# Kernel tuning notes

Hardware: AMD Instinct MI355X
Metric: run time of the kernel (lower is better)

The kernel has to match this reference:

```python
import jax, jax.numpy as jnp
import numpy as np

N = 50000      # nodes
E = 600000     # edges (avg degree 12)
DIN, DE, DH = 17, 1, 128
L, H, C = 3, 4, 32   # layers, heads, per-head channels (DH = H*C)
NEG_SLOPE = 0.2


def setup_inputs() -> dict:
    key = jax.random.key(0)
    ks = jax.random.split(key, 18)
    rn = lambda k, s, sc: jax.random.normal(k, s, jnp.float32) * sc
    return {
        "x": rn(ks[0], (N, DIN), 1.0),
        "edge_index": jax.random.randint(ks[1], (2, E), 0, N, dtype=jnp.int64),
        "edge_attr": rn(ks[2], (E, DE), 1.0),
        "enc_node_w": rn(ks[3], (DIN, DH), 1.0 / np.sqrt(DIN)),
        "enc_node_b": jnp.zeros((DH,), jnp.float32),
        "enc_edge_w": rn(ks[4], (DE, DH), 1.0),
        "enc_edge_b": jnp.zeros((DH,), jnp.float32),
        "lin_w": rn(ks[5], (L, DH, DH), 1.0 / np.sqrt(DH)),
        "lin_edge_w": rn(ks[6], (L, DH, DH), 1.0 / np.sqrt(DH)),
        "att_src": rn(ks[7], (L, H, C), 1.0 / np.sqrt(C)),
        "att_dst": rn(ks[8], (L, H, C), 1.0 / np.sqrt(C)),
        "att_edge": rn(ks[9], (L, H, C), 1.0 / np.sqrt(C)),
        "gat_bias": jnp.zeros((L, DH), jnp.float32),
        "dec_w1": rn(ks[10], (DH, DH), 1.0 / np.sqrt(DH)),
        "dec_b1": jnp.zeros((DH,), jnp.float32),
        "dec_w2": rn(ks[11], (DH, 2), 1.0 / np.sqrt(DH)),
        "dec_b2": jnp.zeros((2,), jnp.float32),
    }


def _gat_layer(x, src, dst, e_attr, W, We, a_src, a_dst, a_edge, bias):
    """PyG GATConv, concat=True, dropout in eval mode (identity).
    x: [N,DH], src/dst: [E2] (self-loops already appended), e_attr: [E2,DH]."""
    n = x.shape[0]
    h = (x @ W).reshape(n, H, C)                       # [N,H,C]
    alpha_src = jnp.einsum('nhc,hc->nh', h, a_src)     # [N,H]
    alpha_dst = jnp.einsum('nhc,hc->nh', h, a_dst)
    e = (e_attr @ We).reshape(-1, H, C)                # [E2,H,C]
    alpha_e = jnp.einsum('ehc,hc->eh', e, a_edge)      # [E2,H]
    logits = jax.nn.leaky_relu(alpha_src[src] + alpha_dst[dst] + alpha_e, NEG_SLOPE)
    # segment softmax over edges grouped by destination node
    mx = jax.ops.segment_max(logits, dst, num_segments=n)          # [N,H]
    num = jnp.exp(logits - mx[dst])                                # [E2,H]
    den = jax.ops.segment_sum(num, dst, num_segments=n)            # [N,H]
    alpha = num / (den[dst] + 1e-16)                               # [E2,H]
    msg = h[src] * alpha[:, :, None]                               # [E2,H,C]
    out = jax.ops.segment_sum(msg, dst, num_segments=n)            # [N,H,C]
    return out.reshape(n, H * C) + bias


def reference(x, edge_index, edge_attr,
              enc_node_w, enc_node_b, enc_edge_w, enc_edge_b,
              lin_w, lin_edge_w, att_src, att_dst, att_edge, gat_bias,
              dec_w1, dec_b1, dec_w2, dec_b2):
    n = x.shape[0]
    src, dst = edge_index[0], edge_index[1]
    h = x @ enc_node_w + enc_node_b                    # node encoder
    ea = edge_attr @ enc_edge_w + enc_edge_b           # edge encoder [E,DH]
    # add_self_loops with fill_value='mean': self-loop attr = mean of incoming edge attrs
    ea_sum = jax.ops.segment_sum(ea, dst, num_segments=n)
    cnt = jax.ops.segment_sum(jnp.ones((ea.shape[0],), ea.dtype), dst, num_segments=n)
    loop_attr = ea_sum / jnp.maximum(cnt, 1.0)[:, None]
    loop_idx = jnp.arange(n, dtype=src.dtype)
    src_f = jnp.concatenate([src, loop_idx])
    dst_f = jnp.concatenate([dst, loop_idx])
    ea_f = jnp.concatenate([ea, loop_attr], axis=0)    # [E+N,DH]
    for l in range(L):
        h = _gat_layer(h, src_f, dst_f, ea_f,
                       lin_w[l], lin_edge_w[l],
                       att_src[l], att_dst[l], att_edge[l], gat_bias[l])
        h = jax.nn.elu(h)
    h = jax.nn.relu(h @ dec_w1 + dec_b1)
    return h @ dec_w2 + dec_b2                          # [N,2]
```

## Files before the change

kernel.cpp:

```cpp
#include <hip/hip_runtime.h>
#include <hip/hip_fp16.h>
#include <math.h>

#define DIN 17
#define DH  128
#define NH  4
#define CC  32
#define NL  3
#define NEG 0.2f

#define CSTRIDE 64

typedef _Float16 hf;
typedef _Float16 f16x8 __attribute__((ext_vector_type(8)));
typedef float    f32x4 __attribute__((ext_vector_type(4)));

#define NT 9

__global__ void __launch_bounds__(256) prep_kernel(
        const float* __restrict__ ew, const float* __restrict__ eb,
        const float* __restrict__ We, const float* __restrict__ ae,
        const float* __restrict__ lin_w, const float* __restrict__ dec_w1,
        const float* __restrict__ att_src, const float* __restrict__ att_dst,
        float* __restrict__ pq, hf* __restrict__ wfrag,
        int* __restrict__ cnt, int N) {
    int b = blockIdx.x, tid = threadIdx.x;
    if (b < 12) {
        if (tid < 64) {
            int l = b >> 2, h = b & 3;
            const float* Wel = We + l * DH * DH;
            const float* ael = ae + l * DH + h * CC;
            float p = 0.f, q = 0.f;
            for (int d = tid; d < DH; d += 64) {
                const float* row = Wel + d * DH + h * CC;
                float wp = 0.f;
                for (int c = 0; c < CC; ++c) wp += row[c] * ael[c];
                p += ew[d] * wp;
                q += eb[d] * wp;
            }
            for (int o = 32; o > 0; o >>= 1) {
                p += __shfl_down(p, o, 64);
                q += __shfl_down(q, o, 64);
            }
            if (tid == 0) { pq[b * 2 + 0] = p; pq[b * 2 + 1] = q; }
        }
    } else if (b < 48) {
        int bb = b - 12;
        int m = bb / NT, nt = bb % NT;
        int lane = tid & 63, kk = tid >> 6;
        int colr = lane & 15, kg = lane >> 4;
        hf* dst = wfrag + ((((size_t)bb * 4 + kk) * 64) + lane) * 8;
        if (nt < 8) {
            const float* src = (m < 3) ? (lin_w + (size_t)m * DH * DH) : dec_w1;
            #pragma unroll
            for (int jj = 0; jj < 8; ++jj) {
                int k = kk * 32 + kg * 8 + jj;
                dst[jj] = (hf)src[k * DH + nt * 16 + colr];
            }
        } else if (m < 3 && colr < 8) {
            int hh = colr >> 1;
            const float* W = lin_w + (size_t)m * DH * DH;
            const float* a = ((colr & 1) ? att_dst : att_src) + m * DH + hh * CC;
            #pragma unroll
            for (int jj = 0; jj < 8; ++jj) {
                int k = kk * 32 + kg * 8 + jj;
                float s = 0.f;
                #pragma unroll
                for (int c = 0; c < CC; ++c) s += W[k * DH + hh * CC + c] * a[c];
                dst[jj] = (hf)s;
            }
        } else {
            #pragma unroll
            for (int jj = 0; jj < 8; ++jj) dst[jj] = (hf)0.f;
        }
    } else {
        int i = (b - 48) * 256 + tid;
        if (i < N) cnt[i] = 0;
    }
}

__global__ void __launch_bounds__(256) rank_enc_kernel(
        const int* __restrict__ ei, const float* __restrict__ ea,
        int* __restrict__ cnt, int2* __restrict__ csr,
        const float* __restrict__ x, const float* __restrict__ Wn,
        const float* __restrict__ bn, hf* __restrict__ h16,
        int E, int N, int EB) {
    __shared__ float wl[DIN][DH];
    __shared__ float xs[32][DIN];
    int tid = threadIdx.x;
    if ((int)blockIdx.x < EB) {
        int e = blockIdx.x * 256 + tid;
        if (e >= E) return;
        int d = ei[E + e];
        int rk = atomicAdd(&cnt[d], 1);
        if (rk < CSTRIDE) {
            int2 p; p.x = ei[e]; p.y = __float_as_int(ea[e]);
            csr[(size_t)d * CSTRIDE + rk] = p;
        }
    } else {
        int row0 = (blockIdx.x - EB) * 32;
        for (int i = tid; i < DIN * DH; i += 256) wl[i / DH][i % DH] = Wn[i];
        for (int i = tid; i < 32 * DIN; i += 256) {
            int r = i / DIN, k = i % DIN;
            int rr = row0 + r; if (rr > N - 1) rr = N - 1;
            xs[r][k] = x[(size_t)rr * DIN + k];
        }
        __syncthreads();
        int c = tid & 127;
        int g = tid >> 7;
        float bias = bn[c];
        #pragma unroll
        for (int r = 0; r < 16; ++r) {
            int row = row0 + g * 16 + r;
            if (row >= N) break;
            float acc = bias;
            #pragma unroll
            for (int k = 0; k < DIN; ++k) acc += xs[g * 16 + r][k] * wl[k][c];
            h16[(size_t)row * DH + c] = (hf)acc;
        }
    }
}

__device__ __forceinline__ void ln_body(
        const hf* __restrict__ h16, const hf* __restrict__ wfrag,
        __half* __restrict__ h1h, float* __restrict__ as_, float* __restrict__ ad_,
        int N, int blk) {
    __shared__ uint4 lds[64 * 16];
    int tid = threadIdx.x;
    int row0 = blk * 64;
    #pragma unroll
    for (int i = 0; i < 4; ++i) {
        int idx = tid + i * 256;
        int r = idx >> 4, ch = idx & 15;
        int gr = row0 + r; if (gr > N - 1) gr = N - 1;
        lds[r * 16 + (ch ^ (r & 7))] = ((const uint4*)(h16 + (size_t)gr * DH))[ch];
    }
    __syncthreads();

    int w = tid >> 6, lane = tid & 63;
    int colr = lane & 15, kg = lane >> 4;
    int lrow = w * 16 + colr;

    f16x8 afr[4];
    #pragma unroll
    for (int kk = 0; kk < 4; ++kk) {
        int ch = (kk * 4 + kg) ^ (colr & 7);
        afr[kk] = *(const f16x8*)&lds[lrow * 16 + ch];
    }

    f32x4 acc[NT];
    #pragma unroll
    for (int nt = 0; nt < NT; ++nt) acc[nt] = (f32x4){0.f, 0.f, 0.f, 0.f};

    const f16x8* wf = (const f16x8*)wfrag;
    #pragma unroll
    for (int nt = 0; nt < NT; ++nt) {
        #pragma unroll
        for (int kk = 0; kk < 4; ++kk) {
            f16x8 bfr = wf[(size_t)(nt * 4 + kk) * 64 + lane];
            acc[nt] = __builtin_amdgcn_mfma_f32_16x16x32_f16(afr[kk], bfr, acc[nt], 0, 0, 0);
        }
    }

    #pragma unroll
    for (int r = 0; r < 4; ++r) {
        int grow = row0 + w * 16 + kg * 4 + r;
        if (grow < N) {
            #pragma unroll
            for (int nt = 0; nt < 8; ++nt)
                h1h[(size_t)grow * DH + nt * 16 + colr] = (__half)(float)acc[nt][r];
        }
    }
    if (colr < 8) {
        int id = colr, hh = id >> 1;
        #pragma unroll
        for (int r = 0; r < 4; ++r) {
            int grow = row0 + w * 16 + kg * 4 + r;
            if (grow < N) {
                float v = (float)acc[8][r];
                if (id & 1) ad_[grow * NH + hh] = v;
                else        as_[grow * NH + hh] = v;
            }
        }
    }
}

__global__ void __launch_bounds__(256) layer_node(
        const hf* __restrict__ h16, const hf* __restrict__ wfrag,
        __half* __restrict__ h1h, float* __restrict__ as_, float* __restrict__ ad_,
        int N) {
    ln_body(h16, wfrag, h1h, as_, ad_, N, blockIdx.x);
}

__global__ void __launch_bounds__(256) agg_kernel(
        const __half* __restrict__ h1h, const float* __restrict__ as_,
        const float* __restrict__ ad_,
        const int* __restrict__ cnt,
        const int2* __restrict__ csr,
        const float* __restrict__ pql, const float* __restrict__ bias,
        hf* __restrict__ hout, int N) {
    int n = blockIdx.x * 4 + (threadIdx.x >> 6);
    if (n >= N) return;
    int lane = threadIdx.x & 63;
    int hd = lane >> 4;
    int c0 = lane * 2;
    size_t off = (size_t)n * CSTRIDE;
    int dgt = cnt[n];
    int dg = dgt < CSTRIDE ? dgt : CSTRIDE;
    float adn = ad_[n * NH + hd];
    float pa = pql[hd * 2 + 0], qa = pql[hd * 2 + 1];

    const __half2* h1v = (const __half2*)h1h;

    float denA = 0.f, a0A = 0.f, a1A = 0.f;
    float denB = 0.f, a0B = 0.f, a1B = 0.f;
    float asv = 0.f;

    int i = 0;
    for (; i + 8 <= dg; i += 8) {
        int2 e[8];
        #pragma unroll
        for (int j = 0; j < 8; ++j) e[j] = csr[off + i + j];
        __half2 q[8];
        #pragma unroll
        for (int j = 0; j < 8; ++j) q[j] = h1v[(size_t)e[j].x * 64 + lane];
        float s[8];
        #pragma unroll
        for (int j = 0; j < 8; ++j) s[j] = as_[e[j].x * NH + hd];
        #pragma unroll
        for (int j = 0; j < 8; ++j) {
            float a = __int_as_float(e[j].y);
            asv += a;
            float t = s[j] + adn + a * pa + qa;
            t = fmaxf(t, NEG * t);
            float nm = __expf(t);
            float2 g = __half22float2(q[j]);
            if (j & 1) { denB += nm; a0B = fmaf(nm, g.x, a0B); a1B = fmaf(nm, g.y, a1B); }
            else       { denA += nm; a0A = fmaf(nm, g.x, a0A); a1A = fmaf(nm, g.y, a1A); }
        }
    }
    for (; i + 4 <= dg; i += 4) {
        int2 e[4];
        #pragma unroll
        for (int j = 0; j < 4; ++j) e[j] = csr[off + i + j];
        __half2 q[4];
        #pragma unroll
        for (int j = 0; j < 4; ++j) q[j] = h1v[(size_t)e[j].x * 64 + lane];
        float s[4];
        #pragma unroll
        for (int j = 0; j < 4; ++j) s[j] = as_[e[j].x * NH + hd];
        #pragma unroll
        for (int j = 0; j < 4; ++j) {
            float a = __int_as_float(e[j].y);
            asv += a;
            float t = s[j] + adn + a * pa + qa;
            t = fmaxf(t, NEG * t);
            float nm = __expf(t);
            float2 g = __half22float2(q[j]);
            if (j & 1) { denB += nm; a0B = fmaf(nm, g.x, a0B); a1B = fmaf(nm, g.y, a1B); }
            else       { denA += nm; a0A = fmaf(nm, g.x, a0A); a1A = fmaf(nm, g.y, a1A); }
        }
    }
    for (; i < dg; ++i) {
        int2 ep = csr[off + i];
        __half2 qs = h1v[(size_t)ep.x * 64 + lane];
        float a = __int_as_float(ep.y);
        asv += a;
        float lg = as_[ep.x * NH + hd] + adn + a * pa + qa;
        lg = fmaxf(lg, NEG * lg);
        float num = __expf(lg);
        float2 gs = __half22float2(qs);
        denA += num;
        a0A = fmaf(num, gs.x, a0A);
        a1A = fmaf(num, gs.y, a1A);
    }

    float sa = asv / fmaxf((float)dgt, 1.f);
    float ael = (dgt > 0) ? (sa * pa + qa) : 0.f;
    float l0 = as_[n * NH + hd] + adn + ael;
    l0 = fmaxf(l0, NEG * l0);
    float numS = __expf(l0);
    float2 hv = __half22float2(h1v[(size_t)n * 64 + lane]);

    float den = denA + denB + numS;
    float a0 = a0A + a0B + numS * hv.x;
    float a1 = a1A + a1B + numS * hv.y;
    float inv = 1.f / (den + 1e-16f);
    float o0 = a0 * inv + bias[c0];
    float o1 = a1 * inv + bias[c0 + 1];
    o0 = (o0 > 0.f) ? o0 : expm1f(o0);
    o1 = (o1 > 0.f) ? o1 : expm1f(o1);
    union { unsigned int u; hf hx[2]; } st;
    st.hx[0] = (hf)o0; st.hx[1] = (hf)o1;
    ((unsigned int*)hout)[(size_t)n * 64 + lane] = st.u;
}

__global__ void __launch_bounds__(256) dec_kernel(
        const hf* __restrict__ h16, const hf* __restrict__ wfrag,
        const float* __restrict__ b1, const float* __restrict__ w2,
        const float* __restrict__ b2, float* __restrict__ out, int N) {
    __shared__ uint4 lds[64 * 16];
    int tid = threadIdx.x;
    int row0 = blockIdx.x * 64;
    #pragma unroll
    for (int i = 0; i < 4; ++i) {
        int idx = tid + i * 256;
        int r = idx >> 4, ch = idx & 15;
        int gr = row0 + r; if (gr > N - 1) gr = N - 1;
        lds[r * 16 + (ch ^ (r & 7))] = ((const uint4*)(h16 + (size_t)gr * DH))[ch];
    }
    __syncthreads();

    int w = tid >> 6, lane = tid & 63;
    int colr = lane & 15, kg = lane >> 4;
    int lrow = w * 16 + colr;

    f16x8 afr[4];
    #pragma unroll
    for (int kk = 0; kk < 4; ++kk) {
        int ch = (kk * 4 + kg) ^ (colr & 7);
        afr[kk] = *(const f16x8*)&lds[lrow * 16 + ch];
    }

    f32x4 acc[8];
    #pragma unroll
    for (int nt = 0; nt < 8; ++nt) acc[nt] = (f32x4){0.f, 0.f, 0.f, 0.f};

    const f16x8* wf = (const f16x8*)wfrag;
    #pragma unroll
    for (int nt = 0; nt < 8; ++nt) {
        #pragma unroll
        for (int kk = 0; kk < 4; ++kk) {
            f16x8 bfr = wf[(size_t)(nt * 4 + kk) * 64 + lane];
            acc[nt] = __builtin_amdgcn_mfma_f32_16x16x32_f16(afr[kk], bfr, acc[nt], 0, 0, 0);
        }
    }

    float bb0 = b2[0], bb1 = b2[1];
    float b1v[8], w20[8], w21[8];
    #pragma unroll
    for (int nt = 0; nt < 8; ++nt) {
        int col = nt * 16 + colr;
        b1v[nt] = b1[col];
        w20[nt] = w2[col * 2 + 0];
        w21[nt] = w2[col * 2 + 1];
    }
    #pragma unroll
    for (int r = 0; r < 4; ++r) {
        float p0 = 0.f, p1 = 0.f;
        #pragma unroll
        for (int nt = 0; nt < 8; ++nt) {
            float hid = fmaxf((float)acc[nt][r] + b1v[nt], 0.f);
            p0 = fmaf(hid, w20[nt], p0);
            p1 = fmaf(hid, w21[nt], p1);
        }
        #pragma unroll
        for (int o = 1; o < 16; o <<= 1) {
            p0 += __shfl_xor(p0, o, 16);
            p1 += __shfl_xor(p1, o, 16);
        }
        int grow = row0 + w * 16 + kg * 4 + r;
        if (colr == 0 && grow < N) {
            out[grow * 2 + 0] = p0 + bb0;
            out[grow * 2 + 1] = p1 + bb1;
        }
    }
}

extern "C" void kernel_launch(void* const* d_in, const int* in_sizes, int n_in,
                              void* d_out, int out_size, void* d_ws, size_t ws_size,
                              hipStream_t stream) {
    const float* x          = (const float*)d_in[0];
    const int*   ei         = (const int*)d_in[1];
    const float* eattr      = (const float*)d_in[2];
    const float* enc_node_w = (const float*)d_in[3];
    const float* enc_node_b = (const float*)d_in[4];
    const float* enc_edge_w = (const float*)d_in[5];
    const float* enc_edge_b = (const float*)d_in[6];
    const float* lin_w      = (const float*)d_in[7];
    const float* lin_edge_w = (const float*)d_in[8];
    const float* att_src    = (const float*)d_in[9];
    const float* att_dst    = (const float*)d_in[10];
    const float* att_edge   = (const float*)d_in[11];
    const float* gat_bias   = (const float*)d_in[12];
    const float* dec_w1     = (const float*)d_in[13];
    const float* dec_b1     = (const float*)d_in[14];
    const float* dec_w2     = (const float*)d_in[15];
    const float* dec_b2     = (const float*)d_in[16];

    const int E = in_sizes[2];
    const int N = in_sizes[0] / DIN;

    char* w = (char*)d_ws;
    auto alloc = [&](size_t bytes) -> void* {
        void* p = (void*)w;
        w += (bytes + 511) & ~((size_t)511);
        return p;
    };
    hf*     h16   = (hf*)alloc((size_t)N * DH * 2);
    __half* h1h   = (__half*)alloc((size_t)N * DH * 2);
    float* as_    = (float*)alloc((size_t)N * NH * 4);
    float* ad_    = (float*)alloc((size_t)N * NH * 4);
    int*   cnt    = (int*)alloc((size_t)N * 4);
    int2*  csr    = (int2*)alloc((size_t)N * CSTRIDE * 8);
    float* pq     = (float*)alloc(NL * NH * 2 * 4);
    hf*    wfrag  = (hf*)alloc((size_t)4 * NT * 4 * 64 * 8 * 2);

    const int EB   = (E + 255) / 256;
    const int NB32 = (N + 31) / 32;
    const int AB   = (N + 255) / 256;
    const int LNB  = (N + 63) / 64;
    const size_t mstride = (size_t)NT * 4 * 64 * 8;

    prep_kernel<<<48 + AB, 256, 0, stream>>>(enc_edge_w, enc_edge_b, lin_edge_w, att_edge,
                                             lin_w, dec_w1, att_src, att_dst,
                                             pq, wfrag, cnt, N);
    rank_enc_kernel<<<EB + NB32, 256, 0, stream>>>(ei, eattr, cnt, csr,
                                                   x, enc_node_w, enc_node_b, h16,
                                                   E, N, EB);
    for (int l = 0; l < NL; ++l) {
        layer_node<<<LNB, 256, 0, stream>>>(h16, wfrag + (size_t)l * mstride,
                                            h1h, as_, ad_, N);
        agg_kernel<<<(N + 3) / 4, 256, 0, stream>>>(h1h, as_, ad_, cnt, csr,
                                                    pq + l * NH * 2, gat_bias + l * DH, h16, N);
    }
    dec_kernel<<<LNB, 256, 0, stream>>>(h16, wfrag + (size_t)3 * mstride,
                                        dec_b1, dec_w2, dec_b2,
                                        (float*)d_out, N);
}
```

Before: 305.4 us.

## Pack CSR entries into 32 bits and fuse prep with edge ranking kernel

Each CSR entry shrinks from an int2 (source index plus fp32 edge attribute) to one 32-bit word: a 16-bit source index and a half-precision edge attribute. This halves CSR traffic in the three aggregation passes. The weight-prep work now runs inside the ranking/encoder kernel, and counter zeroing moves to a small separate kernel. The packing assumes node indices fit in 16 bits, which fails for N=50000 above 65535? No, 50000 fits, and it rounds the edge attribute to fp16.

```diff
diff --git a/kernel.cpp b/kernel.cpp
--- a/kernel.cpp
+++ b/kernel.cpp
@@ -17,17 +17,62 @@
 
 #define NT 9
 
-__global__ void __launch_bounds__(256) prep_kernel(
+union HB { unsigned short us; hf h; };
+
+__global__ void zero_kernel(int* __restrict__ cnt, int N) {
+    int i = blockIdx.x * 256 + threadIdx.x;
+    if (i < N) cnt[i] = 0;
+}
+
+__global__ void __launch_bounds__(256) fused_front(
+        const int* __restrict__ ei, const float* __restrict__ ea,
+        int* __restrict__ cnt, unsigned int* __restrict__ csr,
+        const float* __restrict__ x, const float* __restrict__ Wn,
+        const float* __restrict__ bn, hf* __restrict__ h16,
         const float* __restrict__ ew, const float* __restrict__ eb,
         const float* __restrict__ We, const float* __restrict__ ae,
         const float* __restrict__ lin_w, const float* __restrict__ dec_w1,
         const float* __restrict__ att_src, const float* __restrict__ att_dst,
         float* __restrict__ pq, hf* __restrict__ wfrag,
-        int* __restrict__ cnt, int N) {
+        int E, int N, int EB, int NB32) {
+    __shared__ float wl[DIN][DH];
+    __shared__ float xs[32][DIN];
     int b = blockIdx.x, tid = threadIdx.x;
-    if (b < 12) {
+    if (b < EB) {
+        int e = b * 256 + tid;
+        if (e >= E) return;
+        int d = ei[E + e];
+        int rk = atomicAdd(&cnt[d], 1);
+        if (rk < CSTRIDE) {
+            HB hb; hb.h = (hf)ea[e];
+            unsigned int u = ((unsigned int)hb.us << 16) | (unsigned int)ei[e];
+            csr[(size_t)d * CSTRIDE + rk] = u;
+        }
+    } else if (b < EB + NB32) {
+        int row0 = (b - EB) * 32;
+        for (int i = tid; i < DIN * DH; i += 256) wl[i / DH][i % DH] = Wn[i];
+        for (int i = tid; i < 32 * DIN; i += 256) {
+            int r = i / DIN, k = i % DIN;
+            int rr = row0 + r; if (rr > N - 1) rr = N - 1;
+            xs[r][k] = x[(size_t)rr * DIN + k];
+        }
+        __syncthreads();
+        int c = tid & 127;
+        int g = tid >> 7;
+        float bias = bn[c];
+        #pragma unroll
+        for (int r = 0; r < 16; ++r) {
+            int row = row0 + g * 16 + r;
+            if (row >= N) break;
+            float acc = bias;
+            #pragma unroll
+            for (int k = 0; k < DIN; ++k) acc += xs[g * 16 + r][k] * wl[k][c];
+            h16[(size_t)row * DH + c] = (hf)acc;
+        }
+    } else if (b < EB + NB32 + 12) {
         if (tid < 64) {
-            int l = b >> 2, h = b & 3;
+            int lh = b - EB - NB32;
+            int l = lh >> 2, h = lh & 3;
             const float* Wel = We + l * DH * DH;
             const float* ael = ae + l * DH + h * CC;
             float p = 0.f, q = 0.f;
@@ -42,10 +87,10 @@
                 p += __shfl_down(p, o, 64);
                 q += __shfl_down(q, o, 64);
             }
-            if (tid == 0) { pq[b * 2 + 0] = p; pq[b * 2 + 1] = q; }
-        }
-    } else if (b < 48) {
-        int bb = b - 12;
+            if (tid == 0) { pq[lh * 2 + 0] = p; pq[lh * 2 + 1] = q; }
+        }
+    } else {
+        int bb = b - EB - NB32 - 12;
         int m = bb / NT, nt = bb % NT;
         int lane = tid & 63, kk = tid >> 6;
         int colr = lane & 15, kg = lane >> 4;
@@ -73,51 +118,6 @@
             #pragma unroll
             for (int jj = 0; jj < 8; ++jj) dst[jj] = (hf)0.f;
         }
-    } else {
-        int i = (b - 48) * 256 + tid;
-        if (i < N) cnt[i] = 0;
-    }
-}
-
-__global__ void __launch_bounds__(256) rank_enc_kernel(
-        const int* __restrict__ ei, const float* __restrict__ ea,
-        int* __restrict__ cnt, int2* __restrict__ csr,
-        const float* __restrict__ x, const float* __restrict__ Wn,
-        const float* __restrict__ bn, hf* __restrict__ h16,
-        int E, int N, int EB) {
-    __shared__ float wl[DIN][DH];
-    __shared__ float xs[32][DIN];
-    int tid = threadIdx.x;
-    if ((int)blockIdx.x < EB) {
-        int e = blockIdx.x * 256 + tid;
-        if (e >= E) return;
-        int d = ei[E + e];
-        int rk = atomicAdd(&cnt[d], 1);
-        if (rk < CSTRIDE) {
-            int2 p; p.x = ei[e]; p.y = __float_as_int(ea[e]);
-            csr[(size_t)d * CSTRIDE + rk] = p;
-        }
-    } else {
-        int row0 = (blockIdx.x - EB) * 32;
-        for (int i = tid; i < DIN * DH; i += 256) wl[i / DH][i % DH] = Wn[i];
-        for (int i = tid; i < 32 * DIN; i += 256) {
-            int r = i / DIN, k = i % DIN;
-            int rr = row0 + r; if (rr > N - 1) rr = N - 1;
-            xs[r][k] = x[(size_t)rr * DIN + k];
-        }
-        __syncthreads();
-        int c = tid & 127;
-        int g = tid >> 7;
-        float bias = bn[c];
-        #pragma unroll
-        for (int r = 0; r < 16; ++r) {
-            int row = row0 + g * 16 + r;
-            if (row >= N) break;
-            float acc = bias;
-            #pragma unroll
-            for (int k = 0; k < DIN; ++k) acc += xs[g * 16 + r][k] * wl[k][c];
-            h16[(size_t)row * DH + c] = (hf)acc;
-        }
     }
 }
 
@@ -196,7 +196,7 @@
         const __half* __restrict__ h1h, const float* __restrict__ as_,
         const float* __restrict__ ad_,
         const int* __restrict__ cnt,
-        const int2* __restrict__ csr,
+        const unsigned int* __restrict__ csr,
         const float* __restrict__ pql, const float* __restrict__ bias,
         hf* __restrict__ hout, int N) {
     int n = blockIdx.x * 4 + (threadIdx.x >> 6);
@@ -218,18 +218,19 @@
 
     int i = 0;
     for (; i + 8 <= dg; i += 8) {
-        int2 e[8];
+        unsigned int e[8];
         #pragma unroll
         for (int j = 0; j < 8; ++j) e[j] = csr[off + i + j];
         __half2 q[8];
         #pragma unroll
-        for (int j = 0; j < 8; ++j) q[j] = h1v[(size_t)e[j].x * 64 + lane];
+        for (int j = 0; j < 8; ++j) q[j] = h1v[(size_t)(e[j] & 0xFFFFu) * 64 + lane];
         float s[8];
         #pragma unroll
-        for (int j = 0; j < 8; ++j) s[j] = as_[e[j].x * NH + hd];
+        for (int j = 0; j < 8; ++j) s[j] = as_[(e[j] & 0xFFFFu) * NH + hd];
         #pragma unroll
         for (int j = 0; j < 8; ++j) {
-            float a = __int_as_float(e[j].y);
+            HB hb; hb.us = (unsigned short)(e[j] >> 16);
+            float a = (float)hb.h;
             asv += a;
             float t = s[j] + adn + a * pa + qa;
             t = fmaxf(t, NEG * t);
@@ -240,18 +241,19 @@
         }
     }
     for (; i + 4 <= dg; i += 4) {
-        int2 e[4];
+        unsigned int e[4];
         #pragma unroll
         for (int j = 0; j < 4; ++j) e[j] = csr[off + i + j];
         __half2 q[4];
         #pragma unroll
-        for (int j = 0; j < 4; ++j) q[j] = h1v[(size_t)e[j].x * 64 + lane];
+        for (int j = 0; j < 4; ++j) q[j] = h1v[(size_t)(e[j] & 0xFFFFu) * 64 + lane];
         float s[4];
         #pragma unroll
-        for (int j = 0; j < 4; ++j) s[j] = as_[e[j].x * NH + hd];
+        for (int j = 0; j < 4; ++j) s[j] = as_[(e[j] & 0xFFFFu) * NH + hd];
         #pragma unroll
         for (int j = 0; j < 4; ++j) {
-            float a = __int_as_float(e[j].y);
+            HB hb; hb.us = (unsigned short)(e[j] >> 16);
+            float a = (float)hb.h;
             asv += a;
             float t = s[j] + adn + a * pa + qa;
             t = fmaxf(t, NEG * t);
@@ -262,11 +264,13 @@
         }
     }
     for (; i < dg; ++i) {
-        int2 ep = csr[off + i];
-        __half2 qs = h1v[(size_t)ep.x * 64 + lane];
-        float a = __int_as_float(ep.y);
+        unsigned int eu = csr[off + i];
+        int src = eu & 0xFFFFu;
+        __half2 qs = h1v[(size_t)src * 64 + lane];
+        HB hb; hb.us = (unsigned short)(eu >> 16);
+        float a = (float)hb.h;
         asv += a;
-        float lg = as_[ep.x * NH + hd] + adn + a * pa + qa;
+        float lg = as_[src * NH + hd] + adn + a * pa + qa;
         lg = fmaxf(lg, NEG * lg);
         float num = __expf(lg);
         float2 gs = __half22float2(qs);
@@ -402,7 +406,7 @@
     float* as_    = (float*)alloc((size_t)N * NH * 4);
     float* ad_    = (float*)alloc((size_t)N * NH * 4);
     int*   cnt    = (int*)alloc((size_t)N * 4);
-    int2*  csr    = (int2*)alloc((size_t)N * CSTRIDE * 8);
+    unsigned int* csr = (unsigned int*)alloc((size_t)N * CSTRIDE * 4);
     float* pq     = (float*)alloc(NL * NH * 2 * 4);
     hf*    wfrag  = (hf*)alloc((size_t)4 * NT * 4 * 64 * 8 * 2);
 
@@ -412,12 +416,13 @@
     const int LNB  = (N + 63) / 64;
     const size_t mstride = (size_t)NT * 4 * 64 * 8;
 
-    prep_kernel<<<48 + AB, 256, 0, stream>>>(enc_edge_w, enc_edge_b, lin_edge_w, att_edge,
-                                             lin_w, dec_w1, att_src, att_dst,
-                                             pq, wfrag, cnt, N);
-    rank_enc_kernel<<<EB + NB32, 256, 0, stream>>>(ei, eattr, cnt, csr,
-                                                   x, enc_node_w, enc_node_b, h16,
-                                                   E, N, EB);
+    zero_kernel<<<AB, 256, 0, stream>>>(cnt, N);
+    fused_front<<<EB + NB32 + 48, 256, 0, stream>>>(ei, eattr, cnt, csr,
+                                                    x, enc_node_w, enc_node_b, h16,
+                                                    enc_edge_w, enc_edge_b, lin_edge_w,
+                                                    att_edge, lin_w, dec_w1,
+                                                    att_src, att_dst, pq, wfrag,
+                                                    E, N, EB, NB32);
     for (int l = 0; l < NL; ++l) {
         layer_node<<<LNB, 256, 0, stream>>>(h16, wfrag + (size_t)l * mstride,
                                             h1h, as_, ad_, N);
```

Result: no change. 307.8 us (+0.8%).
